# Performance work log

Measured on AMD Instinct MI355X. Metric: run time of the kernel, lower is better.

## Reference

```python
import jax, jax.numpy as jnp
import numpy as np

B, S, C = 1, 6, 128
Hf, Wf = 56, 100            # feature map (stride-8 of 448x800)
IMG_H, IMG_W = 448, 800
Z, Y, X = 128, 8, 128
BOUNDS = (-50.0, 50.0, -5.0, 5.0, -50.0, 50.0)
CENTROID = (0.0, 0.1, 0.0)
EPS = 1e-6


def _voxel_centers():
    # ref-frame (cam0) coordinates of voxel centers, Vox_util.Mem2Ref of gridcloud3d
    xmin, xmax = BOUNDS[0] + CENTROID[0], BOUNDS[1] + CENTROID[0]
    ymin, ymax = BOUNDS[2] + CENTROID[1], BOUNDS[3] + CENTROID[1]
    zmin, zmax = BOUNDS[4] + CENTROID[2], BOUNDS[5] + CENTROID[2]
    vsx, vsy, vsz = (xmax - xmin) / X, (ymax - ymin) / Y, (zmax - zmin) / Z
    zi, yi, xi = jnp.meshgrid(jnp.arange(Z), jnp.arange(Y), jnp.arange(X), indexing='ij')
    xr = xmin + vsx * 0.5 + xi.astype(jnp.float32) * vsx
    yr = ymin + vsy * 0.5 + yi.astype(jnp.float32) * vsy
    zr = zmin + vsz * 0.5 + zi.astype(jnp.float32) * vsz
    return jnp.stack([xr.reshape(-1), yr.reshape(-1), zr.reshape(-1)], axis=-1)  # (N,3), N=Z*Y*X


def setup_inputs() -> dict:
    key = jax.random.key(0)
    k1, k2 = jax.random.split(key)
    cam_feat = jax.random.normal(k1, (B, S, C, Hf, Wf), dtype=jnp.float32)
    # intrinsics: fx=fy=500, principal point at image center
    K = np.zeros((B, S, 4, 4), np.float32)
    K[..., 0, 0] = 500.0; K[..., 1, 1] = 500.0
    K[..., 0, 2] = IMG_W / 2.0; K[..., 1, 2] = IMG_H / 2.0
    K[..., 2, 2] = 1.0; K[..., 3, 3] = 1.0
    # surround-view rig: rotate about y (camera-frame vertical) by 2*pi*s/S
    ang = np.arange(S) * (2.0 * np.pi / S)
    c, s = np.cos(ang).astype(np.float32), np.sin(ang).astype(np.float32)
    R = np.zeros((B, S, 3, 3), np.float32)
    R[..., 0, 0] = c; R[..., 0, 2] = s; R[..., 1, 1] = 1.0
    R[..., 2, 0] = -s; R[..., 2, 2] = c
    t = np.stack([0.5 * s, np.full(S, -1.0, np.float32), 0.5 * c], axis=-1)[None].astype(np.float32)
    conv_w = jax.random.normal(k2, (C, C * Y, 3, 3), dtype=jnp.float32) * 0.02
    return {
        'cam_feat': cam_feat,
        'intrins': jnp.asarray(K),
        'rots': jnp.asarray(R),
        'trans': jnp.asarray(t),
        'conv_w': conv_w,
    }


def reference(cam_feat, intrins, rots, trans, conv_w):
    Bn, Sn = cam_feat.shape[:2]
    BS = Bn * Sn
    # velo_T_cams = [R|t]; cam0_T_camXs = inv(velo_T_cams[:,0]) @ velo_T_cams
    velo_T = (jnp.zeros((Bn, Sn, 4, 4), cam_feat.dtype)
              .at[..., :3, :3].set(rots)
              .at[..., :3, 3].set(trans)
              .at[..., 3, 3].set(1.0))
    cam0_T_camXs = jnp.einsum('bij,bsjk->bsik', jnp.linalg.inv(velo_T[:, 0]), velo_T)
    camXs_T_cam0 = jnp.linalg.inv(cam0_T_camXs)  # (B,S,4,4)
    # scale_intrinsics to feature resolution
    sx, sy = Wf / float(IMG_W), Hf / float(IMG_H)
    Kf = (jnp.zeros((Bn, Sn, 4, 4), cam_feat.dtype)
          .at[..., 0, 0].set(intrins[..., 0, 0] * sx)
          .at[..., 1, 1].set(intrins[..., 1, 1] * sy)
          .at[..., 0, 2].set(intrins[..., 0, 2] * sx)
          .at[..., 1, 2].set(intrins[..., 1, 2] * sy)
          .at[..., 2, 2].set(1.0).at[..., 3, 3].set(1.0))
    pixB_T_cam0 = jnp.einsum('bsij,bsjk->bsik', Kf, camXs_T_cam0).reshape(BS, 4, 4)
    camXs_T_cam0 = camXs_T_cam0.reshape(BS, 4, 4)

    xyz = _voxel_centers()                                   # (N,3)
    xyz1 = jnp.concatenate([xyz, jnp.ones((xyz.shape[0], 1), xyz.dtype)], axis=-1)  # (N,4)
    cam_pts = jnp.einsum('pij,nj->pni', camXs_T_cam0, xyz1)  # (BS,N,4)
    z = cam_pts[..., 2]
    pix = jnp.einsum('pij,nj->pni', pixB_T_cam0, xyz1)       # (BS,N,4)
    denom = jnp.maximum(pix[..., 2:3], EPS)
    x = pix[..., 0] / denom[..., 0]
    y = pix[..., 1] / denom[..., 0]
    valid = (x > -0.5) & (x < Wf - 0.5) & (y > -0.5) & (y < Hf - 0.5) & (z > 0.0)

    # normalize_grid2d + grid_sample(align_corners=False) unnormalization
    gx = jnp.clip(2.0 * x / (Wf - 1) - 1.0, -2.0, 2.0)
    gy = jnp.clip(2.0 * y / (Hf - 1) - 1.0, -2.0, 2.0)
    ux = ((gx + 1.0) * Wf - 1.0) * 0.5
    uy = ((gy + 1.0) * Hf - 1.0) * 0.5
    x0f, y0f = jnp.floor(ux), jnp.floor(uy)
    wx, wy = ux - x0f, uy - y0f
    x0i, y0i = x0f.astype(jnp.int32), y0f.astype(jnp.int32)

    feat = cam_feat.reshape(BS, C, Hf * Wf)

    def corner(xi, yi, w):
        inb = (xi >= 0) & (xi < Wf) & (yi >= 0) & (yi < Hf)  # zeros padding
        idx = jnp.clip(yi, 0, Hf - 1) * Wf + jnp.clip(xi, 0, Wf - 1)
        v = jnp.take_along_axis(feat, idx[:, None, :], axis=2)  # (BS,C,N)
        return v * (w * inb.astype(w.dtype))[:, None, :]

    vals = (corner(x0i, y0i, (1 - wx) * (1 - wy))
            + corner(x0i + 1, y0i, wx * (1 - wy))
            + corner(x0i, y0i + 1, (1 - wx) * wy)
            + corner(x0i + 1, y0i + 1, wx * wy))
    vals = vals * valid[:, None, :].astype(vals.dtype)
    feat_mems = vals.reshape(Bn, Sn, C, Z, Y, X)

    # reduce_masked_mean over cameras
    mask = (jnp.abs(feat_mems) > 0).astype(feat_mems.dtype)
    feat_mem = jnp.sum(feat_mems * mask, axis=1) / (EPS + jnp.sum(mask, axis=1))  # (B,C,Z,Y,X)

    # BEV compress: permute(0,1,3,2,4) -> (B, C*Y, Z, X), conv3x3 + InstanceNorm + GELU
    bev = jnp.transpose(feat_mem, (0, 1, 3, 2, 4)).reshape(Bn, C * Y, Z, X)
    out = jax.lax.conv_general_dilated(bev, conv_w, (1, 1), 'SAME',
                                       dimension_numbers=('NCHW', 'OIHW', 'NCHW'))
    mu = out.mean(axis=(2, 3), keepdims=True)
    var = out.var(axis=(2, 3), keepdims=True)
    out = (out - mu) * jax.lax.rsqrt(var + 1e-5)
    return jax.nn.gelu(out, approximate=False)
```

## Files before the change

kernel.cpp:

```cpp
#include <hip/hip_runtime.h>
#include <cmath>

#define SNUM 6
#define CNUM 128
#define HF 56
#define WF 100
#define HW (HF*WF)
#define ZN 128
#define YN 8
#define XN 128
#define NVOX (ZN*YN*XN)

typedef __attribute__((ext_vector_type(8))) short bf16x8;
typedef __attribute__((ext_vector_type(4))) float f32x4;
typedef __attribute__((ext_vector_type(4))) int   i32x4;

__device__ __forceinline__ unsigned short f2bf(float f) {
    unsigned u = __builtin_bit_cast(unsigned, f);
    unsigned r = (u + 0x7FFFu + ((u >> 16) & 1u)) >> 16;
    return (unsigned short)r;
}
__device__ __forceinline__ float bf2f(unsigned short h) {
    unsigned u = (unsigned)h << 16;
    return __builtin_bit_cast(float, u);
}

__device__ __forceinline__ void gl_lds16(const void* g, void* l) {
    __builtin_amdgcn_global_load_lds(
        (const __attribute__((address_space(1))) void*)g,
        (__attribute__((address_space(3))) void*)l, 16, 0, 0);
}
__device__ __forceinline__ void gl_lds4(const void* g, void* l) {
    __builtin_amdgcn_global_load_lds(
        (const __attribute__((address_space(1))) void*)g,
        (__attribute__((address_space(3))) void*)l, 4, 0, 0);
}

__global__ void k_setup(const float* __restrict__ intrins,
                        const float* __restrict__ rots,
                        const float* __restrict__ trans,
                        float* __restrict__ mats) {
    int s = threadIdx.x;
    if (s >= SNUM) return;
    float R0[9], Rs[9], t0[3], ts[3];
    for (int i = 0; i < 9; ++i) { R0[i] = rots[i]; Rs[i] = rots[s*9 + i]; }
    for (int i = 0; i < 3; ++i) { t0[i] = trans[i]; ts[i] = trans[s*3 + i]; }
    float M[3][4];
    float d0 = t0[0]-ts[0], d1 = t0[1]-ts[1], d2 = t0[2]-ts[2];
    for (int i = 0; i < 3; ++i) {
        for (int j = 0; j < 3; ++j)
            M[i][j] = Rs[0*3+i]*R0[0*3+j] + Rs[1*3+i]*R0[1*3+j] + Rs[2*3+i]*R0[2*3+j];
        M[i][3] = Rs[0*3+i]*d0 + Rs[1*3+i]*d1 + Rs[2*3+i]*d2;
    }
    const float sx = (float)WF/800.0f, sy = (float)HF/448.0f;
    float fx = intrins[s*16 + 0]*sx, fy = intrins[s*16 + 5]*sy;
    float cx = intrins[s*16 + 2]*sx, cy = intrins[s*16 + 6]*sy;
    float* o = mats + s*24;
    for (int j = 0; j < 4; ++j) {
        o[0*4+j]      = M[0][j];
        o[1*4+j]      = M[1][j];
        o[2*4+j]      = M[2][j];
        o[12 + 0*4+j] = fx*M[0][j] + cx*M[2][j];
        o[12 + 1*4+j] = fy*M[1][j] + cy*M[2][j];
        o[12 + 2*4+j] = M[2][j];
    }
}

__global__ __launch_bounds__(256) void k_tfeat(const float* __restrict__ cf,
                                               unsigned short* __restrict__ featT) {
    __shared__ float t[32][33];
    int s = blockIdx.z;
    int p0 = blockIdx.x * 32, c0 = blockIdx.y * 32;
    int tx = threadIdx.x, ty = threadIdx.y;
#pragma unroll
    for (int k = 0; k < 4; ++k) {
        int r = ty + k*8;
        t[r][tx] = cf[((size_t)s*CNUM + c0 + r)*HW + p0 + tx];
    }
    __syncthreads();
#pragma unroll
    for (int k = 0; k < 4; ++k) {
        int r = ty + k*8;
        featT[((size_t)s*HW + p0 + r)*CNUM + c0 + tx] = f2bf(t[tx][r]);
    }
}

__global__ __launch_bounds__(256) void k_zero(unsigned short* __restrict__ bevin2) {
    int i = blockIdx.x*256 + threadIdx.x;
    if (i >= 66048) return;
    size_t unit;
    if (i < 33280) {
        int zr = i / 16640;
        int j  = i - zr*16640;
        unit = (size_t)(zr ? 129 : 0)*16640 + j;
    } else {
        int j  = i - 33280;
        int zp = 1 + (j >> 8);
        int r  = j & 255;
        int c  = r >> 1;
        int xp = (r & 1) ? 129 : 0;
        unit = ((size_t)zp*128 + c)*130 + xp;
    }
    *(i32x4*)&bevin2[unit*8] = i32x4{0,0,0,0};
}

__global__ __launch_bounds__(256) void k_sample(const unsigned short* __restrict__ featT,
                                                const float* __restrict__ mats,
                                                unsigned short* __restrict__ bevin2) {
#pragma clang fp contract(off)
    __shared__ float xch[16][132];
    __shared__ float2 suv[16][6];
    const int tid = threadIdx.x;
    const int b = blockIdx.x;
    const int z = b >> 6, x0 = (b & 63) * 2;
    const int cl = tid & 15, vs = tid >> 4;
    if (tid < 96) {
        int v = tid / 6, s = tid - (tid/6)*6;
        int yi = v >> 1, xi2 = x0 + (v & 1);
        float xr = -49.609375f + (float)xi2 * 0.78125f;
        float yr = (-4.9f + 0.625f) + (float)yi * 1.25f;
        float zr = -49.609375f + (float)z * 0.78125f;
        const float* m = mats + s*24;
        float zc = m[8]*xr  + m[9]*yr  + m[10]*zr + m[11];
        float ph = m[12]*xr + m[13]*yr + m[14]*zr + m[15];
        float qh = m[16]*xr + m[17]*yr + m[18]*zr + m[19];
        float denom = fmaxf(zc, 1e-6f);
        float px = ph / denom, py = qh / denom;
        bool valid = (px > -0.5f) & (px < (float)WF - 0.5f) &
                     (py > -0.5f) & (py < (float)HF - 0.5f) & (zc > 0.0f);
        float ux = -10000.0f, uy = -10000.0f;
        if (valid) {
            float gx = 2.0f*px/((float)WF - 1.0f) - 1.0f;
            float gy = 2.0f*py/((float)HF - 1.0f) - 1.0f;
            gx = fminf(fmaxf(gx, -2.0f), 2.0f);
            gy = fminf(fmaxf(gy, -2.0f), 2.0f);
            ux = ((gx + 1.0f)*(float)WF - 1.0f)*0.5f;
            uy = ((gy + 1.0f)*(float)HF - 1.0f)*0.5f;
        }
        suv[v][s] = float2{ux, uy};
    }
    __syncthreads();

    const bf16x8 zz8 = {0,0,0,0,0,0,0,0};
    float sum[8], cnt[8];
#pragma unroll
    for (int k = 0; k < 8; ++k) { sum[k] = 0.0f; cnt[k] = 0.0f; }
    for (int s = 0; s < SNUM; ++s) {
        float2 u = suv[vs][s];
        if (u.x < -999.0f) continue;
        float x0f = floorf(u.x), y0f = floorf(u.y);
        float wx = u.x - x0f, wy = u.y - y0f;
        int ix = (int)x0f, iy = (int)y0f;
        float w00 = (1.0f-wx)*(1.0f-wy), w10 = wx*(1.0f-wy);
        float w01 = (1.0f-wx)*wy,        w11 = wx*wy;
        bool bx0 = (ix >= 0) & (ix < WF);
        bool bx1 = (ix >= -1) & (ix < WF-1);
        bool by0 = (iy >= 0) & (iy < HF);
        bool by1 = (iy >= -1) & (iy < HF-1);
        bool c00 = bx0 & by0, c10 = bx1 & by0, c01 = bx0 & by1, c11 = bx1 & by1;
        const unsigned short* fb = featT + (size_t)s * (HW*CNUM) + cl*8;
        long r0 = (long)(iy*WF + ix) * CNUM;
        bf16x8 v00 = c00 ? *(const bf16x8*)(fb + r0)                 : zz8;
        bf16x8 v10 = c10 ? *(const bf16x8*)(fb + r0 + CNUM)          : zz8;
        bf16x8 v01 = c01 ? *(const bf16x8*)(fb + r0 + WF*CNUM)       : zz8;
        bf16x8 v11 = c11 ? *(const bf16x8*)(fb + r0 + WF*CNUM + CNUM): zz8;
#pragma unroll
        for (int k = 0; k < 8; ++k) {
            float v = 0.0f;
            v = v + w00 * bf2f((unsigned short)v00[k]);
            v = v + w10 * bf2f((unsigned short)v10[k]);
            v = v + w01 * bf2f((unsigned short)v01[k]);
            v = v + w11 * bf2f((unsigned short)v11[k]);
            sum[k] += v;
            cnt[k] += (v != 0.0f) ? 1.0f : 0.0f;
        }
    }
#pragma unroll
    for (int k = 0; k < 8; ++k)
        xch[vs][cl*8 + k] = sum[k] / (1e-6f + cnt[k]);
    __syncthreads();
    {
        int c = tid >> 1, xs2 = tid & 1;
        unsigned pk[4];
#pragma unroll
        for (int j = 0; j < 4; ++j) {
            float v0 = xch[(2*j)*2 + xs2][c];
            float v1 = xch[(2*j+1)*2 + xs2][c];
            pk[j] = (unsigned)f2bf(v0) | ((unsigned)f2bf(v1) << 16);
        }
        size_t unit = ((size_t)(z+1)*128 + c)*130 + (x0 + xs2 + 1);
        *(i32x4*)&bevin2[unit*8] = i32x4{(int)pk[0], (int)pk[1], (int)pk[2], (int)pk[3]};
    }
}

__global__ __launch_bounds__(256) void k_wprep(const float* __restrict__ w,
                                               unsigned short* __restrict__ w2) {
    int i = blockIdx.x*256 + threadIdx.x;
    if (i >= 9*128*1024) return;
    int ci = i & 1023; int rest = i >> 10; int co = rest & 127; int tap = rest >> 7;
    w2[i] = f2bf(w[((size_t)co*1024 + ci)*9 + tap]);
}

__global__ __launch_bounds__(256, 1) void k_conv_mfma(
        const unsigned short* __restrict__ bevin2,
        const unsigned short* __restrict__ w2,
        float* __restrict__ out,
        float* __restrict__ psum, float* __restrict__ psq) {
    __shared__ __align__(16) unsigned short lds[2][24*144*8];
    const int tid  = threadIdx.x;
    const int bid  = blockIdx.x;
    const int swz  = (bid & 7)*32 + (bid >> 3);
    const int z0   = swz & 127;
    const int coh  = swz >> 7;
    const int lane = tid & 63, wid = tid >> 6;
    const int wr = wid >> 1, xw = wid & 1;
    const int co_base = coh*64 + wr*32;
    const int l15 = lane & 15, lhi = lane >> 4;

    f32x4 acc[2][4];
#pragma unroll
    for (int f = 0; f < 2; ++f)
#pragma unroll
        for (int nf = 0; nf < 4; ++nf) acc[f][nf] = f32x4{0.f,0.f,0.f,0.f};

    const unsigned short* aw0 = w2 + ((size_t)(co_base      + l15))*1024 + lhi*8;
    const unsigned short* aw1 = w2 + ((size_t)(co_base + 16 + l15))*1024 + lhi*8;

    bf16x8 aC[12], aN[12];

#define STAGE(BUF, STEP)                                                       \
    {                                                                          \
        _Pragma("unroll")                                                      \
        for (int r6 = 0; r6 < 6; ++r6) {                                       \
            int r = wid*6 + r6;                                                \
            int zrel = r >> 3, cq = r & 7;                                     \
            const unsigned short* gsrc = bevin2 +                              \
                (((size_t)(z0 + zrel)*128 + (STEP)*8 + cq)*130)*8;             \
            unsigned short* ldst = &lds[BUF][r*144*8];                         \
            gl_lds16(gsrc + (size_t)lane*8, ldst);                             \
            gl_lds16(gsrc + (size_t)(64 + lane)*8, ldst + 64*8);               \
            gl_lds4 (gsrc + 128*8 + (size_t)lane*2, ldst + 128*8);             \
        }                                                                      \
    }
#define A12(DST, DZ, CI0)                                                      \
    {                                                                          \
        _Pragma("unroll")                                                      \
        for (int t = 0; t < 3; ++t)                                            \
            _Pragma("unroll")                                                  \
            for (int ks = 0; ks < 2; ++ks) {                                   \
                DST[(t*2+ks)*2+0] = *(const bf16x8*)(aw0 + (size_t)((DZ)*3+t)*131072 + (CI0) + ks*32); \
                DST[(t*2+ks)*2+1] = *(const bf16x8*)(aw1 + (size_t)((DZ)*3+t)*131072 + (CI0) + ks*32); \
            }                                                                  \
    }
#define CDZ(DZ, BUF, AFR)                                                      \
    {                                                                          \
        __builtin_amdgcn_s_setprio(1);                                         \
        _Pragma("unroll")                                                      \
        for (int dx = 0; dx < 3; ++dx)                                         \
            _Pragma("unroll")                                                  \
            for (int ks = 0; ks < 2; ++ks) {                                   \
                bf16x8 a0 = AFR[(dx*2+ks)*2+0];                                \
                bf16x8 a1 = AFR[(dx*2+ks)*2+1];                                \
                _Pragma("unroll")                                              \
                for (int nf = 0; nf < 4; ++nf) {                               \
                    bf16x8 bfr = *(const bf16x8*)&lds[BUF][(((DZ)*8 + ks*4 + lhi)*144 + xw*64 + nf*16 + l15 + dx)*8]; \
                    acc[0][nf] = __builtin_amdgcn_mfma_f32_16x16x32_bf16(a0, bfr, acc[0][nf], 0, 0, 0); \
                    acc[1][nf] = __builtin_amdgcn_mfma_f32_16x16x32_bf16(a1, bfr, acc[1][nf], 0, 0, 0); \
                }                                                              \
            }                                                                  \
        __builtin_amdgcn_s_setprio(0);                                         \
    }

    STAGE(0, 0);
    A12(aC, 0, 0);
    __syncthreads();

    for (int cc = 0; cc < 8; ++cc) {
        const int s0 = 2*cc;
        STAGE(1, s0 + 1);
        A12(aN, 1, s0*64);        CDZ(0, 0, aC);
        A12(aC, 2, s0*64);        CDZ(1, 0, aN);
        A12(aN, 0, (s0+1)*64);    CDZ(2, 0, aC);
        __syncthreads();
        if (cc < 7) STAGE(0, s0 + 2);
        A12(aC, 1, (s0+1)*64);    CDZ(0, 1, aN);
        A12(aN, 2, (s0+1)*64);    CDZ(1, 1, aC);
        if (cc < 7) A12(aC, 0, (s0+2)*64);
        CDZ(2, 1, aN);
        if (cc < 7) __syncthreads();
    }

    float ps[2][4], pq[2][4];
#pragma unroll
    for (int f = 0; f < 2; ++f)
#pragma unroll
        for (int r = 0; r < 4; ++r) { ps[f][r] = 0.0f; pq[f][r] = 0.0f; }
#pragma unroll
    for (int f = 0; f < 2; ++f)
#pragma unroll
        for (int nf = 0; nf < 4; ++nf)
#pragma unroll
            for (int r = 0; r < 4; ++r) {
                int co = co_base + f*16 + lhi*4 + r;
                float v = acc[f][nf][r];
                out[(size_t)co*16384 + z0*128 + xw*64 + nf*16 + l15] = v;
                ps[f][r] += v;
                pq[f][r] += v*v;
            }
#pragma unroll
    for (int f = 0; f < 2; ++f)
#pragma unroll
        for (int r = 0; r < 4; ++r) {
            float s = ps[f][r], q = pq[f][r];
#pragma unroll
            for (int m = 1; m < 16; m <<= 1) {
                s += __shfl_xor(s, m);
                q += __shfl_xor(q, m);
            }
            if (l15 == 0) {
                int co = co_base + f*16 + lhi*4 + r;
                int pb = z0*2 + xw;
                psum[co*256 + pb] = s;
                psq [co*256 + pb] = q;
            }
        }
#undef STAGE
#undef A12
#undef CDZ
}

__global__ __launch_bounds__(256) void k_stats(const float* __restrict__ psum,
                                               const float* __restrict__ psq,
                                               float* __restrict__ stats) {
    __shared__ float r1[256], r2[256];
    int co = blockIdx.x, tid = threadIdx.x;
    r1[tid] = psum[co*256 + tid];
    r2[tid] = psq [co*256 + tid];
    __syncthreads();
    for (int off = 128; off > 0; off >>= 1) {
        if (tid < off) { r1[tid] += r1[tid+off]; r2[tid] += r2[tid+off]; }
        __syncthreads();
    }
    if (tid == 0) {
        float mean = r1[0] * (1.0f/16384.0f);
        float var  = r2[0] * (1.0f/16384.0f) - mean*mean;
        stats[co*2]   = mean;
        stats[co*2+1] = rsqrtf(var + 1e-5f);
    }
}

__global__ __launch_bounds__(256) void k_gelu(float* __restrict__ out,
                                              const float* __restrict__ stats) {
    int i = blockIdx.x*256 + threadIdx.x;
    int co = i >> 14;
    float v = out[i];
    float r = (v - stats[co*2]) * stats[co*2+1];
    out[i] = 0.5f * r * (1.0f + erff(r * 0.70710678118654752f));
}

extern "C" void kernel_launch(void* const* d_in, const int* in_sizes, int n_in,
                              void* d_out, int out_size, void* d_ws, size_t ws_size,
                              hipStream_t stream) {
    const float* cam_feat = (const float*)d_in[0];
    const float* intrins  = (const float*)d_in[1];
    const float* rots     = (const float*)d_in[2];
    const float* trans    = (const float*)d_in[3];
    const float* conv_w   = (const float*)d_in[4];
    float* out = (float*)d_out;
    float* ws  = (float*)d_ws;

    float* mats  = ws;
    unsigned short* featT  = (unsigned short*)(ws + 160);
    unsigned short* bevin2 = featT + (size_t)SNUM*HW*CNUM;
    unsigned short* w2     = bevin2 + (size_t)130*128*130*8;
    float* psum  = (float*)(w2 + 9*128*1024);
    float* psq   = psum + 32768;
    float* stats = psq + 32768;

    hipLaunchKernelGGL(k_setup, dim3(1), dim3(64), 0, stream, intrins, rots, trans, mats);
    hipLaunchKernelGGL(k_tfeat, dim3(HW/32, CNUM/32, SNUM), dim3(32,8), 0, stream, cam_feat, featT);
    hipLaunchKernelGGL(k_wprep, dim3((9*128*1024 + 255)/256), dim3(256), 0, stream, conv_w, w2);
    hipLaunchKernelGGL(k_zero, dim3((66048 + 255)/256), dim3(256), 0, stream, bevin2);
    hipLaunchKernelGGL(k_sample, dim3(8192), dim3(256), 0, stream, featT, mats, bevin2);
    hipLaunchKernelGGL(k_conv_mfma, dim3(256), dim3(256), 0, stream, bevin2, w2, out, psum, psq);
    hipLaunchKernelGGL(k_stats, dim3(128), dim3(256), 0, stream, psum, psq, stats);
    hipLaunchKernelGGL(k_gelu, dim3(8192), dim3(256), 0, stream, out, stats);
}
```

Measured before the change: 138.9 us.

## Fuse instance-norm stats and GELU into conv via cooperative grid sync

```diff
diff --git a/kernel.cpp b/kernel.cpp
--- a/kernel.cpp
+++ b/kernel.cpp
@@ -1,5 +1,8 @@
 #include <hip/hip_runtime.h>
+#include <hip/hip_cooperative_groups.h>
 #include <cmath>
+
+namespace cg = cooperative_groups;
 
 #define SNUM 6
 #define CNUM 128
@@ -201,12 +204,13 @@
     w2[i] = f2bf(w[((size_t)co*1024 + ci)*9 + tap]);
 }
 
-__global__ __launch_bounds__(256, 1) void k_conv_mfma(
+__global__ __launch_bounds__(256, 1) void k_conv_fused(
         const unsigned short* __restrict__ bevin2,
         const unsigned short* __restrict__ w2,
         float* __restrict__ out,
         float* __restrict__ psum, float* __restrict__ psq) {
     __shared__ __align__(16) unsigned short lds[2][24*144*8];
+    __shared__ float smean[64], srstd[64];
     const int tid  = threadIdx.x;
     const int bid  = blockIdx.x;
     const int swz  = (bid & 7)*32 + (bid >> 3);
@@ -254,7 +258,6 @@
     }
 #define CDZ(DZ, BUF, AFR)                                                      \
     {                                                                          \
-        __builtin_amdgcn_s_setprio(1);                                         \
         _Pragma("unroll")                                                      \
         for (int dx = 0; dx < 3; ++dx)                                         \
             _Pragma("unroll")                                                  \
@@ -268,7 +271,6 @@
                     acc[1][nf] = __builtin_amdgcn_mfma_f32_16x16x32_bf16(a1, bfr, acc[1][nf], 0, 0, 0); \
                 }                                                              \
             }                                                                  \
-        __builtin_amdgcn_s_setprio(0);                                         \
     }
 
     STAGE(0, 0);
@@ -290,72 +292,77 @@
         if (cc < 7) __syncthreads();
     }
 
-    float ps[2][4], pq[2][4];
+    {
+        float ps[2][4], pq[2][4];
+#pragma unroll
+        for (int f = 0; f < 2; ++f)
+#pragma unroll
+            for (int r = 0; r < 4; ++r) { ps[f][r] = 0.0f; pq[f][r] = 0.0f; }
+#pragma unroll
+        for (int f = 0; f < 2; ++f)
+#pragma unroll
+            for (int nf = 0; nf < 4; ++nf)
+#pragma unroll
+                for (int r = 0; r < 4; ++r) {
+                    float v = acc[f][nf][r];
+                    ps[f][r] += v;
+                    pq[f][r] += v*v;
+                }
+#pragma unroll
+        for (int f = 0; f < 2; ++f)
+#pragma unroll
+            for (int r = 0; r < 4; ++r) {
+                float s = ps[f][r], q = pq[f][r];
+#pragma unroll
+                for (int m = 1; m < 16; m <<= 1) {
+                    s += __shfl_xor(s, m);
+                    q += __shfl_xor(q, m);
+                }
+                if (l15 == 0) {
+                    int co = co_base + f*16 + lhi*4 + r;
+                    int pb = z0*2 + xw;
+                    psum[co*256 + pb] = s;
+                    psq [co*256 + pb] = q;
+                }
+            }
+    }
+    __threadfence();
+    cg::this_grid().sync();
+
+    {
+        int col = tid >> 2, q = tid & 3;
+        int co = coh*64 + col;
+        float s = 0.0f, qq = 0.0f;
+        const float* pp = psum + co*256 + q*64;
+        const float* pg = psq  + co*256 + q*64;
+#pragma unroll 8
+        for (int j = 0; j < 64; ++j) { s += pp[j]; qq += pg[j]; }
+        s  += __shfl_xor(s, 1);  qq += __shfl_xor(qq, 1);
+        s  += __shfl_xor(s, 2);  qq += __shfl_xor(qq, 2);
+        if (q == 0) {
+            float mean = s * (1.0f/16384.0f);
+            float var  = qq * (1.0f/16384.0f) - mean*mean;
+            smean[col] = mean;
+            srstd[col] = rsqrtf(var + 1e-5f);
+        }
+    }
+    __syncthreads();
+
 #pragma unroll
     for (int f = 0; f < 2; ++f)
 #pragma unroll
-        for (int r = 0; r < 4; ++r) { ps[f][r] = 0.0f; pq[f][r] = 0.0f; }
-#pragma unroll
-    for (int f = 0; f < 2; ++f)
-#pragma unroll
         for (int nf = 0; nf < 4; ++nf)
 #pragma unroll
             for (int r = 0; r < 4; ++r) {
-                int co = co_base + f*16 + lhi*4 + r;
+                int col = wr*32 + f*16 + lhi*4 + r;
                 float v = acc[f][nf][r];
-                out[(size_t)co*16384 + z0*128 + xw*64 + nf*16 + l15] = v;
-                ps[f][r] += v;
-                pq[f][r] += v*v;
+                float rr = (v - smean[col]) * srstd[col];
+                float g = 0.5f * rr * (1.0f + erff(rr * 0.70710678118654752f));
+                out[(size_t)(coh*64 + col)*16384 + z0*128 + xw*64 + nf*16 + l15] = g;
             }
-#pragma unroll
-    for (int f = 0; f < 2; ++f)
-#pragma unroll
-        for (int r = 0; r < 4; ++r) {
-            float s = ps[f][r], q = pq[f][r];
-#pragma unroll
-            for (int m = 1; m < 16; m <<= 1) {
-                s += __shfl_xor(s, m);
-                q += __shfl_xor(q, m);
-            }
-            if (l15 == 0) {
-                int co = co_base + f*16 + lhi*4 + r;
-                int pb = z0*2 + xw;
-                psum[co*256 + pb] = s;
-                psq [co*256 + pb] = q;
-            }
-        }
 #undef STAGE
 #undef A12
 #undef CDZ
-}
-
-__global__ __launch_bounds__(256) void k_stats(const float* __restrict__ psum,
-                                               const float* __restrict__ psq,
-                                               float* __restrict__ stats) {
-    __shared__ float r1[256], r2[256];
-    int co = blockIdx.x, tid = threadIdx.x;
-    r1[tid] = psum[co*256 + tid];
-    r2[tid] = psq [co*256 + tid];
-    __syncthreads();
-    for (int off = 128; off > 0; off >>= 1) {
-        if (tid < off) { r1[tid] += r1[tid+off]; r2[tid] += r2[tid+off]; }
-        __syncthreads();
-    }
-    if (tid == 0) {
-        float mean = r1[0] * (1.0f/16384.0f);
-        float var  = r2[0] * (1.0f/16384.0f) - mean*mean;
-        stats[co*2]   = mean;
-        stats[co*2+1] = rsqrtf(var + 1e-5f);
-    }
-}
-
-__global__ __launch_bounds__(256) void k_gelu(float* __restrict__ out,
-                                              const float* __restrict__ stats) {
-    int i = blockIdx.x*256 + threadIdx.x;
-    int co = i >> 14;
-    float v = out[i];
-    float r = (v - stats[co*2]) * stats[co*2+1];
-    out[i] = 0.5f * r * (1.0f + erff(r * 0.70710678118654752f));
 }
 
 extern "C" void kernel_launch(void* const* d_in, const int* in_sizes, int n_in,
@@ -375,14 +382,19 @@
     unsigned short* w2     = bevin2 + (size_t)130*128*130*8;
     float* psum  = (float*)(w2 + 9*128*1024);
     float* psq   = psum + 32768;
-    float* stats = psq + 32768;
 
     hipLaunchKernelGGL(k_setup, dim3(1), dim3(64), 0, stream, intrins, rots, trans, mats);
     hipLaunchKernelGGL(k_tfeat, dim3(HW/32, CNUM/32, SNUM), dim3(32,8), 0, stream, cam_feat, featT);
     hipLaunchKernelGGL(k_wprep, dim3((9*128*1024 + 255)/256), dim3(256), 0, stream, conv_w, w2);
     hipLaunchKernelGGL(k_zero, dim3((66048 + 255)/256), dim3(256), 0, stream, bevin2);
     hipLaunchKernelGGL(k_sample, dim3(8192), dim3(256), 0, stream, featT, mats, bevin2);
-    hipLaunchKernelGGL(k_conv_mfma, dim3(256), dim3(256), 0, stream, bevin2, w2, out, psum, psq);
-    hipLaunchKernelGGL(k_stats, dim3(128), dim3(256), 0, stream, psum, psq, stats);
-    hipLaunchKernelGGL(k_gelu, dim3(8192), dim3(256), 0, stream, out, stats);
-}
+
+    {
+        const unsigned short* a0 = bevin2;
+        const unsigned short* a1 = w2;
+        float* a2 = out; float* a3 = psum; float* a4 = psq;
+        void* args[5] = { (void*)&a0, (void*)&a1, (void*)&a2, (void*)&a3, (void*)&a4 };
+        hipLaunchCooperativeKernel((const void*)k_conv_fused,
+                                   dim3(256), dim3(256), args, 0, stream);
+    }
+}
```

New measurement: 224.7 us. 61.8% more time.

## Use 4-deep LDS ring with vmcnt waits in MFMA BEV conv

Applied to the files above, without the earlier changes.

```diff
diff --git a/kernel.cpp b/kernel.cpp
--- a/kernel.cpp
+++ b/kernel.cpp
@@ -206,7 +206,7 @@
         const unsigned short* __restrict__ w2,
         float* __restrict__ out,
         float* __restrict__ psum, float* __restrict__ psq) {
-    __shared__ __align__(16) unsigned short lds[2][24*144*8];
+    __shared__ __align__(16) unsigned short lds[4][12*144*8];
     const int tid  = threadIdx.x;
     const int bid  = blockIdx.x;
     const int swz  = (bid & 7)*32 + (bid >> 3);
@@ -226,68 +226,64 @@
     const unsigned short* aw0 = w2 + ((size_t)(co_base      + l15))*1024 + lhi*8;
     const unsigned short* aw1 = w2 + ((size_t)(co_base + 16 + l15))*1024 + lhi*8;
 
-    bf16x8 aC[12], aN[12];
-
-#define STAGE(BUF, STEP)                                                       \
+    bf16x8 aC[6], aN[6];
+
+#define STAGE(STEP)                                                            \
     {                                                                          \
         _Pragma("unroll")                                                      \
-        for (int r6 = 0; r6 < 6; ++r6) {                                       \
-            int r = wid*6 + r6;                                                \
-            int zrel = r >> 3, cq = r & 7;                                     \
+        for (int r3 = 0; r3 < 3; ++r3) {                                       \
+            int r = wid*3 + r3;                                                \
+            int zrel = r >> 2, cq = r & 3;                                     \
             const unsigned short* gsrc = bevin2 +                              \
-                (((size_t)(z0 + zrel)*128 + (STEP)*8 + cq)*130)*8;             \
-            unsigned short* ldst = &lds[BUF][r*144*8];                         \
+                (((size_t)(z0 + zrel)*128 + (STEP)*4 + cq)*130)*8;             \
+            unsigned short* ldst = &lds[(STEP) & 3][r*144*8];                  \
             gl_lds16(gsrc + (size_t)lane*8, ldst);                             \
             gl_lds16(gsrc + (size_t)(64 + lane)*8, ldst + 64*8);               \
             gl_lds4 (gsrc + 128*8 + (size_t)lane*2, ldst + 128*8);             \
         }                                                                      \
     }
-#define A12(DST, DZ, CI0)                                                      \
+#define A6(DST, DZ, CI0)                                                       \
     {                                                                          \
         _Pragma("unroll")                                                      \
-        for (int t = 0; t < 3; ++t)                                            \
-            _Pragma("unroll")                                                  \
-            for (int ks = 0; ks < 2; ++ks) {                                   \
-                DST[(t*2+ks)*2+0] = *(const bf16x8*)(aw0 + (size_t)((DZ)*3+t)*131072 + (CI0) + ks*32); \
-                DST[(t*2+ks)*2+1] = *(const bf16x8*)(aw1 + (size_t)((DZ)*3+t)*131072 + (CI0) + ks*32); \
-            }                                                                  \
+        for (int t = 0; t < 3; ++t) {                                          \
+            DST[t*2+0] = *(const bf16x8*)(aw0 + (size_t)((DZ)*3+t)*131072 + (CI0)); \
+            DST[t*2+1] = *(const bf16x8*)(aw1 + (size_t)((DZ)*3+t)*131072 + (CI0)); \
+        }                                                                      \
     }
 #define CDZ(DZ, BUF, AFR)                                                      \
     {                                                                          \
-        __builtin_amdgcn_s_setprio(1);                                         \
         _Pragma("unroll")                                                      \
-        for (int dx = 0; dx < 3; ++dx)                                         \
+        for (int dx = 0; dx < 3; ++dx) {                                       \
+            bf16x8 a0 = AFR[dx*2+0];                                           \
+            bf16x8 a1 = AFR[dx*2+1];                                           \
             _Pragma("unroll")                                                  \
-            for (int ks = 0; ks < 2; ++ks) {                                   \
-                bf16x8 a0 = AFR[(dx*2+ks)*2+0];                                \
-                bf16x8 a1 = AFR[(dx*2+ks)*2+1];                                \
-                _Pragma("unroll")                                              \
-                for (int nf = 0; nf < 4; ++nf) {                               \
-                    bf16x8 bfr = *(const bf16x8*)&lds[BUF][(((DZ)*8 + ks*4 + lhi)*144 + xw*64 + nf*16 + l15 + dx)*8]; \
-                    acc[0][nf] = __builtin_amdgcn_mfma_f32_16x16x32_bf16(a0, bfr, acc[0][nf], 0, 0, 0); \
-                    acc[1][nf] = __builtin_amdgcn_mfma_f32_16x16x32_bf16(a1, bfr, acc[1][nf], 0, 0, 0); \
-                }                                                              \
+            for (int nf = 0; nf < 4; ++nf) {                                   \
+                bf16x8 bfr = *(const bf16x8*)&lds[BUF][(((DZ)*4 + lhi)*144 + xw*64 + nf*16 + l15 + dx)*8]; \
+                acc[0][nf] = __builtin_amdgcn_mfma_f32_16x16x32_bf16(a0, bfr, acc[0][nf], 0, 0, 0); \
+                acc[1][nf] = __builtin_amdgcn_mfma_f32_16x16x32_bf16(a1, bfr, acc[1][nf], 0, 0, 0); \
             }                                                                  \
-        __builtin_amdgcn_s_setprio(0);                                         \
-    }
-
-    STAGE(0, 0);
-    A12(aC, 0, 0);
-    __syncthreads();
-
-    for (int cc = 0; cc < 8; ++cc) {
-        const int s0 = 2*cc;
-        STAGE(1, s0 + 1);
-        A12(aN, 1, s0*64);        CDZ(0, 0, aC);
-        A12(aC, 2, s0*64);        CDZ(1, 0, aN);
-        A12(aN, 0, (s0+1)*64);    CDZ(2, 0, aC);
-        __syncthreads();
-        if (cc < 7) STAGE(0, s0 + 2);
-        A12(aC, 1, (s0+1)*64);    CDZ(0, 1, aN);
-        A12(aN, 2, (s0+1)*64);    CDZ(1, 1, aC);
-        if (cc < 7) A12(aC, 0, (s0+2)*64);
-        CDZ(2, 1, aN);
-        if (cc < 7) __syncthreads();
+        }                                                                      \
+    }
+#define PIPE_WAIT()  asm volatile("s_waitcnt vmcnt(24)" ::: "memory")
+
+    STAGE(0); STAGE(1); STAGE(2);
+    A6(aC, 0, 0);
+
+    for (int p = 0; p < 16; ++p) {
+        const int s = 2*p;
+        PIPE_WAIT();
+        __builtin_amdgcn_s_barrier();
+        if (s + 3 < 32) STAGE(s + 3);
+        A6(aN, 1, s*32);          CDZ(0, (s & 3), aC);
+        A6(aC, 2, s*32);          CDZ(1, (s & 3), aN);
+        A6(aN, 0, (s+1)*32);      CDZ(2, (s & 3), aC);
+        PIPE_WAIT();
+        __builtin_amdgcn_s_barrier();
+        if (s + 4 < 32) STAGE(s + 4);
+        A6(aC, 1, (s+1)*32);      CDZ(0, ((s+1) & 3), aN);
+        A6(aN, 2, (s+1)*32);      CDZ(1, ((s+1) & 3), aC);
+        if (s + 2 < 32) A6(aC, 0, (s+2)*32);
+        CDZ(2, ((s+1) & 3), aN);
     }
 
     float ps[2][4], pq[2][4];
@@ -325,8 +321,9 @@
             }
         }
 #undef STAGE
-#undef A12
+#undef A6
 #undef CDZ
+#undef PIPE_WAIT
 }
 
 __global__ __launch_bounds__(256) void k_stats(const float* __restrict__ psum,
```

Result: slower. 155.8 us (+12.2%).
